# Kernel optimization log

Hardware: AMD Instinct MI355X
Metric: run time of the kernel (lower is better)

The kernel has to match this reference:

```python
import jax, jax.numpy as jnp
import numpy as np

NUM_HEADS = 6
DIM = 192
WS = (2, 6, 12)          # window size (z, h, w)
DATA = (8, 96, 180)      # padded (plev, lat, lon)
SHIFT = (1, 3, 6)


def _position_index(ws):
    Z, H, W = ws
    zi, zj = np.arange(Z), -np.arange(Z) * Z
    hi, hj = np.arange(H), -np.arange(H) * H
    w = np.arange(W)
    c1 = np.stack(np.meshgrid(zi, hi, w, indexing='ij')).reshape(3, -1)
    c2 = np.stack(np.meshgrid(zj, hj, w, indexing='ij')).reshape(3, -1)
    coords = (c1[:, :, None] - c2[:, None, :]).transpose(1, 2, 0).copy()
    coords[:, :, 2] += W - 1
    coords[:, :, 1] *= 2 * W - 1
    coords[:, :, 0] *= (2 * W - 1) * H * H
    return coords.sum(-1).reshape(-1).astype(np.int32)


def _shift_mask(data, ws, ss):
    Z, H, W = data
    img = np.zeros((Z, H, W))
    cnt = 0
    for z in ((0, -ss[0]), (-ss[0], None)):
        for h in ((0, -ss[1]), (-ss[1], None)):
            for w in ((0, None),):  # lam=False: longitude is cyclic, no w split
                img[z[0]:z[1], h[0]:h[1], w[0]:w[1]] = cnt
                cnt += 1
    m = img.reshape(Z // ws[0], ws[0], H // ws[1], ws[1], W // ws[2], ws[2])
    m = m.transpose(0, 2, 4, 1, 3, 5).reshape(-1, ws[0] * ws[1] * ws[2])
    diff = m[:, None, :] - m[:, :, None]
    return np.where(diff != 0, -100.0, 0.0).astype(np.float32)


def setup_inputs() -> dict:
    key = jax.random.key(0)
    ks = jax.random.split(key, 4)
    N = WS[0] * WS[1] * WS[2]                      # 144 tokens / window
    nW = (DATA[0] // WS[0]) * (DATA[1] // WS[1])   # 64 (z,h) window pairs
    wlon = DATA[2] // WS[2]                        # 15 lon windows
    B_ = 1 * nW * wlon                             # 960 total windows (batch=1)
    bias_rows = (2 * WS[2] - 1) * WS[1] ** 2 * WS[0] ** 2  # 3312
    return {
        'x': jax.random.normal(ks[0], (B_, N, DIM), jnp.float32),
        'w1': jax.random.normal(ks[1], (DIM, 3 * DIM), jnp.float32) * 0.02,
        'b1': jnp.zeros((3 * DIM,), jnp.float32),
        'w2': jax.random.normal(ks[2], (DIM, DIM), jnp.float32) * 0.02,
        'b2': jnp.zeros((DIM,), jnp.float32),
        'bias_table': jax.random.normal(ks[3], (bias_rows, nW, NUM_HEADS), jnp.float32) * 0.02,
        'mask': jnp.asarray(_shift_mask(DATA, WS, SHIFT)),
        'position_index': jnp.asarray(_position_index(WS)),
        'batch_size': 1,
    }


def reference(x, w1, b1, w2, b2, bias_table, mask, position_index, batch_size):
    B_, N, C = x.shape
    Ch = C // NUM_HEADS
    scale = Ch ** -0.5
    qkv = (x @ w1 + b1).reshape(B_, N, 3, NUM_HEADS, Ch)
    qkv = jnp.transpose(qkv, (2, 0, 3, 1, 4))      # (3, B_, H, N, Ch)
    q, k, v = qkv[0] * scale, qkv[1], qkv[2]
    attn = jnp.einsum('bhnc,bhmc->bhnm', q, k)      # (B_, H, N, N)
    nW = bias_table.shape[1]
    wlon = B_ // (batch_size * nW)
    # earth-specific bias gather: (N*N,) -> (nW, H, N, N)
    bias = bias_table[position_index].reshape(N, N, nW, NUM_HEADS)
    bias = jnp.transpose(bias, (2, 3, 0, 1))
    attn = attn.reshape(batch_size, nW, wlon, NUM_HEADS, N, N) + bias[None, :, None]
    # shift mask add: (total_windows, N, N) broadcast over batch and heads
    attn = attn.reshape(batch_size, nW * wlon, NUM_HEADS, N, N) + mask[None, :, None]
    attn = jax.nn.softmax(attn.reshape(B_, NUM_HEADS, N, N), axis=-1)
    out = jnp.einsum('bhnm,bhmc->bnhc', attn, v).reshape(B_, N, C)
    return out @ w2 + b2
```

## Files before the change

kernel.cpp:

```cpp
#include <hip/hip_runtime.h>

typedef __attribute__((ext_vector_type(8))) short bf16x8;
typedef __attribute__((ext_vector_type(4))) float f32x4;
typedef unsigned short u16;
typedef unsigned int u32;

#define NTOK 144
#define CDIM 192
#define NH 6
#define CH 32
#define C3 576
#define NWIN 64
#define WLON 15
#define SCALE 0.17677669529663687f
#define LOG2E 1.4426950408889634f

#define OFF_W1T  0u
#define OFF_W2T  221184u
#define OFF_COMB 294912u
#define OFF_Q    32145408u
#define OFF_K    85229568u
#define OFF_V    138313728u

__device__ __forceinline__ u16 f2b(float f){
  u32 u = __float_as_uint(f);
  u32 r = u + 0x7FFFu + ((u >> 16) & 1u);
  return (u16)(r >> 16);
}
__device__ __forceinline__ u32 pk2(float a, float b){
  return (u32)f2b(a) | ((u32)f2b(b) << 16);
}

extern "C" __global__ __launch_bounds__(256) void prep_weights(
    const float* __restrict__ w1, const float* __restrict__ w2,
    u16* __restrict__ w1t, u16* __restrict__ w2t){
  int idx = blockIdx.x * 256 + threadIdx.x;
  if (idx < CDIM * C3){ int k = idx / C3;  int c = idx - k * C3;  w1t[c * CDIM + k] = f2b(w1[idx]); }
  if (idx < CDIM * CDIM){ int k = idx / CDIM; int c = idx - k * CDIM; w2t[c * CDIM + k] = f2b(w2[idx]); }
}

extern "C" __global__ __launch_bounds__(192) void prep_comb(
    const float* __restrict__ bt, const float* __restrict__ mask,
    const int* __restrict__ pidx, float* __restrict__ comb){
  int nwh = blockIdx.x;
  int nw = nwh / NH, h = nwh - nw * NH;
  int tl = blockIdx.y * 192 + threadIdx.x;
  int ti = tl / 576;
  int rem = tl - ti * 576;
  int nt = rem >> 6, lane = rem & 63;
  int ib = ti * 16 + ((lane >> 4) << 2);
  int j  = nt * 16 + (lane & 15);
  const float* mrow = mask + (size_t)(nw * WLON) * (NTOK * NTOK);
  float4 v;
  float* vp = reinterpret_cast<float*>(&v);
  #pragma unroll
  for (int r = 0; r < 4; ++r){
    int e = (ib + r) * NTOK + j;
    int pi = pidx[e];
    vp[r] = (bt[((size_t)pi * NWIN + nw) * NH + h] + mrow[e]) * LOG2E;
  }
  *reinterpret_cast<float4*>(comb + ((size_t)nwh * 5184 + tl) * 4) = v;
}

#define BPAD 200
extern "C" __global__ __launch_bounds__(256, 3) void qkv_gemm(
    const float* __restrict__ x, const u16* __restrict__ w1t, const float* __restrict__ b1,
    u16* __restrict__ qw, u16* __restrict__ kw, u16* __restrict__ vw){
  __shared__ u16 Bl[2][64 * BPAD];
  const int tid = threadIdx.x;
  const int wid = tid >> 6, lane = tid & 63, l15 = lane & 15, l4 = lane >> 4;
  const size_t row0 = (size_t)blockIdx.x * 128 + wid * 32;
  const f32x4 zz = {0.f, 0.f, 0.f, 0.f};

  bf16x8 af[2][6];
  #pragma unroll
  for (int mf = 0; mf < 2; ++mf){
    const float* src = x + (row0 + mf * 16 + l15) * CDIM + l4 * 8;
    #pragma unroll
    for (int kk = 0; kk < 6; ++kk){
      float4 f0 = *reinterpret_cast<const float4*>(src + kk * 32);
      float4 f1 = *reinterpret_cast<const float4*>(src + kk * 32 + 4);
      union { bf16x8 v; uint4 u; } cv;
      cv.u.x = pk2(f0.x, f0.y); cv.u.y = pk2(f0.z, f0.w);
      cv.u.z = pk2(f1.x, f1.y); cv.u.w = pk2(f1.z, f1.w);
      af[mf][kk] = cv.v;
    }
  }
  int bw_[2], n0_[2];
  #pragma unroll
  for (int mf = 0; mf < 2; ++mf){
    int t0 = (int)row0 + mf * 16 + l4 * 4;
    bw_[mf] = t0 / NTOK; n0_[mf] = t0 - bw_[mf] * NTOK;
  }

  const int sr = tid >> 2, sq = tid & 3;
  {
    const u16* src = w1t + (size_t)sr * CDIM + sq * 48;
    u16* dst = &Bl[0][sr * BPAD + sq * 48];
    #pragma unroll
    for (int i = 0; i < 48; i += 8)
      *reinterpret_cast<uint4*>(dst + i) = *reinterpret_cast<const uint4*>(src + i);
  }

  int cur = 0;
  #pragma unroll 1
  for (int nt = 0; nt < 9; ++nt){
    __syncthreads();
    if (nt < 8){
      const u16* src = w1t + (size_t)((nt + 1) * 64 + sr) * CDIM + sq * 48;
      u16* dst = &Bl[cur ^ 1][sr * BPAD + sq * 48];
      #pragma unroll
      for (int i = 0; i < 48; i += 8)
        *reinterpret_cast<uint4*>(dst + i) = *reinterpret_cast<const uint4*>(src + i);
    }
    f32x4 acc[2][4];
    #pragma unroll
    for (int mf = 0; mf < 2; ++mf)
      #pragma unroll
      for (int nf = 0; nf < 4; ++nf) acc[mf][nf] = zz;
    #pragma unroll
    for (int kk = 0; kk < 6; ++kk){
      bf16x8 bfr[4];
      #pragma unroll
      for (int nf = 0; nf < 4; ++nf)
        bfr[nf] = *reinterpret_cast<const bf16x8*>(&Bl[cur][(nf * 16 + l15) * BPAD + kk * 32 + l4 * 8]);
      #pragma unroll
      for (int mf = 0; mf < 2; ++mf)
        #pragma unroll
        for (int nf = 0; nf < 4; ++nf)
          acc[mf][nf] = __builtin_amdgcn_mfma_f32_16x16x32_bf16(af[mf][kk], bfr[nf], acc[mf][nf], 0, 0, 0);
    }
    int which = nt / 3;
    #pragma unroll
    for (int nf = 0; nf < 4; ++nf){
      int c = nt * 64 + nf * 16 + l15;
      int rem = c - which * CDIM;
      int hh = rem >> 5, chh = rem & 31;
      float bias = b1[c];
      if (which == 2){
        #pragma unroll
        for (int mf = 0; mf < 2; ++mf){
          uint2 pv;
          pv.x = pk2(acc[mf][nf][0] + bias, acc[mf][nf][1] + bias);
          pv.y = pk2(acc[mf][nf][2] + bias, acc[mf][nf][3] + bias);
          *reinterpret_cast<uint2*>(vw + (((size_t)bw_[mf] * NH + hh) * CH + chh) * NTOK + n0_[mf]) = pv;
        }
      } else {
        u16* base = (which == 0) ? qw : kw;
        float mult = (which == 0) ? (SCALE * LOG2E) : 1.0f;
        #pragma unroll
        for (int mf = 0; mf < 2; ++mf)
          #pragma unroll
          for (int r = 0; r < 4; ++r)
            base[(((size_t)bw_[mf] * NH + hh) * NTOK + n0_[mf] + r) * CH + chh] = f2b((acc[mf][nf][r] + bias) * mult);
      }
    }
    cur ^= 1;
  }
}

extern "C" __global__ __launch_bounds__(512, 4) void attn_kernel(
    const u16* __restrict__ qw, const u16* __restrict__ kw, const u16* __restrict__ vw,
    const float* __restrict__ comb, float* __restrict__ outbuf){
  __shared__ u16 Pl[8][16][40];
  const int tid = threadIdx.x;
  const int wv = tid >> 6, lane = tid & 63, l15 = lane & 15, l4 = lane >> 4;
  const int gw = blockIdx.x * 8 + wv;
  const int b = gw / NH, h = gw - b * NH;
  const size_t qkbase = ((size_t)b * NH + h) * (NTOK * CH);
  const size_t vbase  = ((size_t)b * NH + h) * (CH * NTOK);
  const float* cb = comb + ((size_t)((b / WLON) * NH + h)) * (5184 * 4);
  u16* Pw = &Pl[wv][0][0];
  u16* stash = reinterpret_cast<u16*>(outbuf);
  const f32x4 zz = {0.f, 0.f, 0.f, 0.f};

  bf16x8 bk[9];
  #pragma unroll
  for (int nt = 0; nt < 9; ++nt)
    bk[nt] = *reinterpret_cast<const bf16x8*>(kw + qkbase + (nt * 16 + l15) * CH + l4 * 8);

  #pragma unroll 1
  for (int ti = 0; ti < 9; ++ti){
    bf16x8 aq = *reinterpret_cast<const bf16x8*>(qw + qkbase + (ti * 16 + l15) * CH + l4 * 8);
    f32x4 s[9];
    #pragma unroll
    for (int nt = 0; nt < 9; ++nt){
      f32x4 cf = *reinterpret_cast<const f32x4*>(cb + ((size_t)(ti * 9 + nt) * 64 + lane) * 4);
      s[nt] = __builtin_amdgcn_mfma_f32_16x16x32_bf16(aq, bk[nt], cf, 0, 0, 0);
    }
    float invs[4];
    #pragma unroll
    for (int r = 0; r < 4; ++r){
      float sum = 0.f;
      #pragma unroll
      for (int nt = 0; nt < 9; ++nt){
        float p = exp2f(s[nt][r]);
        s[nt][r] = p; sum += p;
      }
      #pragma unroll
      for (int off = 8; off; off >>= 1) sum += __shfl_xor(sum, off, 16);
      invs[r] = 1.0f / sum;
    }
    f32x4 o0 = zz, o1 = zz;
    #pragma unroll
    for (int kk = 0; kk < 5; ++kk){
      #pragma unroll
      for (int r = 0; r < 4; ++r){
        Pw[(l4 * 4 + r) * 40 + l15] = f2b(s[2 * kk][r]);
        if (kk < 4) Pw[(l4 * 4 + r) * 40 + 16 + l15] = f2b(s[2 * kk + 1][r]);
      }
      int j0 = kk * 32 + l4 * 8;
      int jc = (j0 < NTOK) ? j0 : 0;
      bf16x8 ap = *reinterpret_cast<const bf16x8*>(Pw + l15 * 40 + l4 * 8);
      bf16x8 bv0 = *reinterpret_cast<const bf16x8*>(vw + vbase + (size_t)l15 * NTOK + jc);
      bf16x8 bv1 = *reinterpret_cast<const bf16x8*>(vw + vbase + (size_t)(16 + l15) * NTOK + jc);
      if (j0 >= NTOK) ap = bf16x8{0, 0, 0, 0, 0, 0, 0, 0};
      o0 = __builtin_amdgcn_mfma_f32_16x16x32_bf16(ap, bv0, o0, 0, 0, 0);
      o1 = __builtin_amdgcn_mfma_f32_16x16x32_bf16(ap, bv1, o1, 0, 0, 0);
    }
    #pragma unroll
    for (int r = 0; r < 4; ++r){
      size_t t = (size_t)b * NTOK + ti * 16 + l4 * 4 + r;
      float is = invs[r];
      stash[t * 384 + 192 + h * CH + l15]      = f2b(o0[r] * is);
      stash[t * 384 + 192 + h * CH + 16 + l15] = f2b(o1[r] * is);
    }
  }
}

extern "C" __global__ __launch_bounds__(256, 2) void proj_gemm(
    const u16* __restrict__ w2t, const float* __restrict__ b2, float* __restrict__ outbuf){
  const int tid = threadIdx.x;
  const int wid = tid >> 6, lane = tid & 63, l15 = lane & 15, l4 = lane >> 4;
  const int hb = blockIdx.y;
  const f32x4 zz = {0.f, 0.f, 0.f, 0.f};

  bf16x8 bfr[6][6];
  #pragma unroll
  for (int nf = 0; nf < 6; ++nf)
    #pragma unroll
    for (int kk = 0; kk < 6; ++kk)
      bfr[nf][kk] = *reinterpret_cast<const bf16x8*>(
          w2t + (size_t)(hb * 96 + nf * 16 + l15) * CDIM + kk * 32 + l4 * 8);

  const u16* stash = reinterpret_cast<const u16*>(outbuf);
  const size_t rbase = (size_t)blockIdx.x * 256 + wid * 64;

#define LOADA(dst, mt) { \
    const u16* src_ = stash + (rbase + (mt) * 16 + l15) * 384 + 192 + l4 * 8; \
    _Pragma("unroll") \
    for (int kk = 0; kk < 6; ++kk) dst[kk] = *reinterpret_cast<const bf16x8*>(src_ + kk * 32); }

#define COMPUTE(a_, mt) { \
    f32x4 acc[6]; \
    _Pragma("unroll") \
    for (int nf = 0; nf < 6; ++nf) acc[nf] = zz; \
    _Pragma("unroll") \
    for (int kk = 0; kk < 6; ++kk) \
      _Pragma("unroll") \
      for (int nf = 0; nf < 6; ++nf) \
        acc[nf] = __builtin_amdgcn_mfma_f32_16x16x32_bf16(a_[kk], bfr[nf][kk], acc[nf], 0, 0, 0); \
    _Pragma("unroll") \
    for (int nf = 0; nf < 6; ++nf){ \
      int c = hb * 96 + nf * 16 + l15; \
      float bias = b2[c]; \
      _Pragma("unroll") \
      for (int r = 0; r < 4; ++r) \
        outbuf[(rbase + (mt) * 16 + l4 * 4 + r) * CDIM + c] = acc[nf][r] + bias; } }

  bf16x8 a0[6], a1[6];
  LOADA(a0, 0)
  LOADA(a1, 1) COMPUTE(a0, 0)
  LOADA(a0, 2) COMPUTE(a1, 1)
  LOADA(a1, 3) COMPUTE(a0, 2)
  COMPUTE(a1, 3)
#undef LOADA
#undef COMPUTE
}

extern "C" void kernel_launch(void* const* d_in, const int* in_sizes, int n_in,
                              void* d_out, int out_size, void* d_ws, size_t ws_size,
                              hipStream_t stream){
  const float* x    = (const float*)d_in[0];
  const float* w1   = (const float*)d_in[1];
  const float* b1   = (const float*)d_in[2];
  const float* w2   = (const float*)d_in[3];
  const float* b2   = (const float*)d_in[4];
  const float* bt   = (const float*)d_in[5];
  const float* mask = (const float*)d_in[6];
  const int*   pidx = (const int*)d_in[7];
  (void)in_sizes; (void)n_in; (void)out_size; (void)ws_size;

  char* ws = (char*)d_ws;
  u16*   w1t  = (u16*)(ws + OFF_W1T);
  u16*   w2t  = (u16*)(ws + OFF_W2T);
  float* comb = (float*)(ws + OFF_COMB);
  u16*   qw   = (u16*)(ws + OFF_Q);
  u16*   kw   = (u16*)(ws + OFF_K);
  u16*   vw   = (u16*)(ws + OFF_V);
  float* out = (float*)d_out;

  prep_weights<<<dim3(432), dim3(256), 0, stream>>>(w1, w2, w1t, w2t);
  prep_comb<<<dim3(384, 27), dim3(192), 0, stream>>>(bt, mask, pidx, comb);
  qkv_gemm<<<dim3(1080), dim3(256), 0, stream>>>(x, w1t, b1, qw, kw, vw);
  attn_kernel<<<dim3(720), dim3(512), 0, stream>>>(qw, kw, vw, comb, out);
  proj_gemm<<<dim3(540, 2), dim3(256), 0, stream>>>(w2t, b2, out);
}
```

Baseline: 291.1 us.

## Store bias+mask table in bf16, prefetch it, and pack attention output stores

The combined bias+mask table is now written in bf16 instead of fp32, which halves its footprint and the bandwidth the attention kernel spends reading it. The attention kernel software-prefetches the next row-tile's bias fragments into registers while computing the current one. K fragments are reloaded inside the loop instead of being held resident, and the occupancy hint is dropped. The V columns are interleaved even/odd so each lane writes its two output channels as one packed 32-bit store. Bias values lose precision in bf16, and the register and occupancy balance changes.

```diff
diff --git a/kernel.cpp b/kernel.cpp
--- a/kernel.cpp
+++ b/kernel.cpp
@@ -18,9 +18,9 @@
 #define OFF_W1T  0u
 #define OFF_W2T  221184u
 #define OFF_COMB 294912u
-#define OFF_Q    32145408u
-#define OFF_K    85229568u
-#define OFF_V    138313728u
+#define OFF_Q    16220160u
+#define OFF_K    69304320u
+#define OFF_V    122388480u
 
 __device__ __forceinline__ u16 f2b(float f){
   u32 u = __float_as_uint(f);
@@ -41,7 +41,7 @@
 
 extern "C" __global__ __launch_bounds__(192) void prep_comb(
     const float* __restrict__ bt, const float* __restrict__ mask,
-    const int* __restrict__ pidx, float* __restrict__ comb){
+    const int* __restrict__ pidx, u16* __restrict__ comb){
   int nwh = blockIdx.x;
   int nw = nwh / NH, h = nwh - nw * NH;
   int tl = blockIdx.y * 192 + threadIdx.x;
@@ -51,15 +51,15 @@
   int ib = ti * 16 + ((lane >> 4) << 2);
   int j  = nt * 16 + (lane & 15);
   const float* mrow = mask + (size_t)(nw * WLON) * (NTOK * NTOK);
-  float4 v;
-  float* vp = reinterpret_cast<float*>(&v);
+  float v[4];
   #pragma unroll
   for (int r = 0; r < 4; ++r){
     int e = (ib + r) * NTOK + j;
     int pi = pidx[e];
-    vp[r] = (bt[((size_t)pi * NWIN + nw) * NH + h] + mrow[e]) * LOG2E;
-  }
-  *reinterpret_cast<float4*>(comb + ((size_t)nwh * 5184 + tl) * 4) = v;
+    v[r] = (bt[((size_t)pi * NWIN + nw) * NH + h] + mrow[e]) * LOG2E;
+  }
+  uint2 out; out.x = pk2(v[0], v[1]); out.y = pk2(v[2], v[3]);
+  *reinterpret_cast<uint2*>(comb + ((size_t)nwh * 5184 + tl) * 4) = out;
 }
 
 #define BPAD 200
@@ -159,9 +159,9 @@
   }
 }
 
-extern "C" __global__ __launch_bounds__(512, 4) void attn_kernel(
+extern "C" __global__ __launch_bounds__(512) void attn_kernel(
     const u16* __restrict__ qw, const u16* __restrict__ kw, const u16* __restrict__ vw,
-    const float* __restrict__ comb, float* __restrict__ outbuf){
+    const u16* __restrict__ comb, float* __restrict__ outbuf){
   __shared__ u16 Pl[8][16][40];
   const int tid = threadIdx.x;
   const int wv = tid >> 6, lane = tid & 63, l15 = lane & 15, l4 = lane >> 4;
@@ -169,24 +169,35 @@
   const int b = gw / NH, h = gw - b * NH;
   const size_t qkbase = ((size_t)b * NH + h) * (NTOK * CH);
   const size_t vbase  = ((size_t)b * NH + h) * (CH * NTOK);
-  const float* cb = comb + ((size_t)((b / WLON) * NH + h)) * (5184 * 4);
+  const u16* cb = comb + ((size_t)((b / WLON) * NH + h)) * (5184 * 4);
   u16* Pw = &Pl[wv][0][0];
-  u16* stash = reinterpret_cast<u16*>(outbuf);
+  u32* stash32 = reinterpret_cast<u32*>(outbuf);
   const f32x4 zz = {0.f, 0.f, 0.f, 0.f};
 
-  bf16x8 bk[9];
+  uint2 cc[9];
   #pragma unroll
   for (int nt = 0; nt < 9; ++nt)
-    bk[nt] = *reinterpret_cast<const bf16x8*>(kw + qkbase + (nt * 16 + l15) * CH + l4 * 8);
+    cc[nt] = *reinterpret_cast<const uint2*>(cb + ((size_t)nt * 64 + lane) * 4);
 
   #pragma unroll 1
   for (int ti = 0; ti < 9; ++ti){
+    const int tin = (ti < 8) ? ti + 1 : ti;
+    uint2 ccn[9];
+    #pragma unroll
+    for (int nt = 0; nt < 9; ++nt)
+      ccn[nt] = *reinterpret_cast<const uint2*>(cb + ((size_t)(tin * 9 + nt) * 64 + lane) * 4);
+
     bf16x8 aq = *reinterpret_cast<const bf16x8*>(qw + qkbase + (ti * 16 + l15) * CH + l4 * 8);
     f32x4 s[9];
     #pragma unroll
     for (int nt = 0; nt < 9; ++nt){
-      f32x4 cf = *reinterpret_cast<const f32x4*>(cb + ((size_t)(ti * 9 + nt) * 64 + lane) * 4);
-      s[nt] = __builtin_amdgcn_mfma_f32_16x16x32_bf16(aq, bk[nt], cf, 0, 0, 0);
+      f32x4 cf;
+      cf[0] = __uint_as_float(cc[nt].x << 16);
+      cf[1] = __uint_as_float(cc[nt].x & 0xFFFF0000u);
+      cf[2] = __uint_as_float(cc[nt].y << 16);
+      cf[3] = __uint_as_float(cc[nt].y & 0xFFFF0000u);
+      bf16x8 bk = *reinterpret_cast<const bf16x8*>(kw + qkbase + (nt * 16 + l15) * CH + l4 * 8);
+      s[nt] = __builtin_amdgcn_mfma_f32_16x16x32_bf16(aq, bk, cf, 0, 0, 0);
     }
     float invs[4];
     #pragma unroll
@@ -201,7 +212,7 @@
       for (int off = 8; off; off >>= 1) sum += __shfl_xor(sum, off, 16);
       invs[r] = 1.0f / sum;
     }
-    f32x4 o0 = zz, o1 = zz;
+    f32x4 oe = zz, oo = zz;
     #pragma unroll
     for (int kk = 0; kk < 5; ++kk){
       #pragma unroll
@@ -212,19 +223,20 @@
       int j0 = kk * 32 + l4 * 8;
       int jc = (j0 < NTOK) ? j0 : 0;
       bf16x8 ap = *reinterpret_cast<const bf16x8*>(Pw + l15 * 40 + l4 * 8);
-      bf16x8 bv0 = *reinterpret_cast<const bf16x8*>(vw + vbase + (size_t)l15 * NTOK + jc);
-      bf16x8 bv1 = *reinterpret_cast<const bf16x8*>(vw + vbase + (size_t)(16 + l15) * NTOK + jc);
+      bf16x8 bve = *reinterpret_cast<const bf16x8*>(vw + vbase + (size_t)(2 * l15) * NTOK + jc);
+      bf16x8 bvo = *reinterpret_cast<const bf16x8*>(vw + vbase + (size_t)(2 * l15 + 1) * NTOK + jc);
       if (j0 >= NTOK) ap = bf16x8{0, 0, 0, 0, 0, 0, 0, 0};
-      o0 = __builtin_amdgcn_mfma_f32_16x16x32_bf16(ap, bv0, o0, 0, 0, 0);
-      o1 = __builtin_amdgcn_mfma_f32_16x16x32_bf16(ap, bv1, o1, 0, 0, 0);
+      oe = __builtin_amdgcn_mfma_f32_16x16x32_bf16(ap, bve, oe, 0, 0, 0);
+      oo = __builtin_amdgcn_mfma_f32_16x16x32_bf16(ap, bvo, oo, 0, 0, 0);
     }
     #pragma unroll
     for (int r = 0; r < 4; ++r){
       size_t t = (size_t)b * NTOK + ti * 16 + l4 * 4 + r;
       float is = invs[r];
-      stash[t * 384 + 192 + h * CH + l15]      = f2b(o0[r] * is);
-      stash[t * 384 + 192 + h * CH + 16 + l15] = f2b(o1[r] * is);
-    }
+      stash32[t * 192 + 96 + h * 16 + l15] = pk2(oe[r] * is, oo[r] * is);
+    }
+    #pragma unroll
+    for (int nt = 0; nt < 9; ++nt) cc[nt] = ccn[nt];
   }
 }
 
@@ -294,7 +306,7 @@
   char* ws = (char*)d_ws;
   u16*   w1t  = (u16*)(ws + OFF_W1T);
   u16*   w2t  = (u16*)(ws + OFF_W2T);
-  float* comb = (float*)(ws + OFF_COMB);
+  u16*   comb = (u16*)(ws + OFF_COMB);
   u16*   qw   = (u16*)(ws + OFF_Q);
   u16*   kw   = (u16*)(ws + OFF_K);
   u16*   vw   = (u16*)(ws + OFF_V);
```

Measured after the change: 247.2 us. 1.18x faster.
